# Optimization experiments

Hardware: AMD Instinct MI355X
Metric: run time of the kernel (lower is better)

Reference implementation:

```python
import jax, jax.numpy as jnp
import numpy as np

CH, KS, PAD = 64, 3, 1
B, H, W = 4, 128, 128
EH, EW = 64, 64
K = KS * KS


def setup_inputs() -> dict:
    key = jax.random.key(0)
    ks = jax.random.split(key, 10)
    C = CH
    z = lambda *s: jnp.zeros(s, jnp.float32)
    return {
        "ev_feat": jax.random.normal(ks[0], (B, C, EH, EW), jnp.float32),
        "im_feat": jax.random.normal(ks[1], (B, C, H, W), jnp.float32),
        "mlp_w0": jax.random.normal(ks[2], (2 * C + 4, C), jnp.float32) * 0.05,
        "mlp_b0": z(C),
        "mlp_w1": jax.random.normal(ks[3], (C, C), jnp.float32) * 0.05,
        "mlp_b1": z(C),
        "mlp_w2": jax.random.normal(ks[4], (C, C), jnp.float32) * 0.05,
        "mlp_b2": z(C),
        "mlp_w3": jax.random.normal(ks[5], (C, C), jnp.float32) * 0.05,
        "mlp_b3": z(C),
        "off_w": jax.random.normal(ks[6], (3 * K, C, KS, KS), jnp.float32) * 0.01,
        "off_b": z(3 * K),
        "dcn_w": jax.random.normal(ks[7], (C, C, KS, KS), jnp.float32) * 0.05,
        "dcn_b": z(C),
    }


def _conv(x, w, b):
    y = jax.lax.conv_general_dilated(x, w, (1, 1), [(PAD, PAD), (PAD, PAD)],
                                     dimension_numbers=("NCHW", "OIHW", "NCHW"))
    return y + b[None, :, None, None]


def _forward(ev_feat, im_feat, mlp_w0, mlp_b0, mlp_w1, mlp_b1, mlp_w2, mlp_b2,
             mlp_w3, mlp_b3, off_w, off_b, dcn_w, dcn_b):
    C = CH
    Bn = im_feat.shape[0]
    Q = H * W
    # ---- coordinate-conditioned MLP: LIIF-style nearest query of ev_feat ----
    ys = -1.0 + (2.0 * jnp.arange(H, dtype=jnp.float32) + 1.0) / H  # pixel centers in [-1,1]
    xs = -1.0 + (2.0 * jnp.arange(W, dtype=jnp.float32) + 1.0) / W
    gy, gx = jnp.meshgrid(ys, xs, indexing="ij")
    coord = jnp.stack([gy, gx], -1).reshape(-1, 2)  # (Q,2) as (y,x), torch make_coord order
    iy = jnp.clip(jnp.round(((coord[:, 0] + 1.0) * EH - 1.0) / 2.0), 0, EH - 1).astype(jnp.int32)
    ix = jnp.clip(jnp.round(((coord[:, 1] + 1.0) * EW - 1.0) / 2.0), 0, EW - 1).astype(jnp.int32)
    q_feat = ev_feat[:, :, iy, ix].transpose(0, 2, 1)  # (B,Q,C) nearest-sampled event feature
    q_coord = jnp.stack([-1.0 + (2.0 * iy + 1.0) / EH, -1.0 + (2.0 * ix + 1.0) / EW], -1)
    rel = (coord - q_coord) * jnp.array([EH, EW], jnp.float32)  # (Q,2) rel coord scaled by feat res
    rel_cell = jnp.array([2.0 / H * EH, 2.0 / W * EW], jnp.float32)  # cell * feat res
    q_im = im_feat.reshape(Bn, C, Q).transpose(0, 2, 1)  # (B,Q,C); coords are im_feat pixel centers
    inp = jnp.concatenate([q_feat, q_im,
                           jnp.broadcast_to(rel, (Bn, Q, 2)),
                           jnp.broadcast_to(rel_cell, (Bn, Q, 2))], -1)  # (B,Q,2C+4)
    x = jax.nn.relu(inp @ mlp_w0 + mlp_b0)
    x = jax.nn.relu(x @ mlp_w1 + mlp_b1)
    x = jax.nn.relu(x @ mlp_w2 + mlp_b2)
    x = x @ mlp_w3 + mlp_b3  # (B,Q,C)
    feat = x.reshape(Bn, H, W, C).transpose(0, 3, 1, 2)  # (B,C,H,W)
    # ---- ModulatedDeformConvPack (DCNv2) ----
    oo = _conv(feat, off_w, off_b)  # (B,3K,H,W)
    o1, o2, m = oo[:, :K], oo[:, K:2 * K], oo[:, 2 * K:]
    off = jnp.concatenate([o1, o2], 1)  # (B,2K,H,W), interleaved (y,x) per kernel tap
    off_y, off_x = off[:, 0::2], off[:, 1::2]  # (B,K,H,W)
    mask = jax.nn.sigmoid(m)  # (B,K,H,W)
    ky = (jnp.arange(K) // KS - PAD).astype(jnp.float32)
    kx = (jnp.arange(K) % KS - PAD).astype(jnp.float32)
    py = jnp.arange(H, dtype=jnp.float32)[None, :, None] + ky[:, None, None] + off_y  # (B,K,H,W)
    px = jnp.arange(W, dtype=jnp.float32)[None, None, :] + kx[:, None, None] + off_x
    y0 = jnp.floor(py)
    x0 = jnp.floor(px)
    ly = py - y0
    lx = px - x0

    def gather(yi, xi):
        valid = (yi >= 0) & (yi <= H - 1) & (xi >= 0) & (xi <= W - 1)
        yc = jnp.clip(yi, 0, H - 1).astype(jnp.int32)
        xc = jnp.clip(xi, 0, W - 1).astype(jnp.int32)
        v = jax.vmap(lambda img, yy, xx: img[:, yy, xx])(feat, yc, xc)  # (B,C,K,H,W)
        return v * valid[:, None].astype(feat.dtype)

    w00 = ((1 - ly) * (1 - lx))[:, None]
    w01 = ((1 - ly) * lx)[:, None]
    w10 = (ly * (1 - lx))[:, None]
    w11 = (ly * lx)[:, None]
    samp = (gather(y0, x0) * w00 + gather(y0, x0 + 1) * w01 +
            gather(y0 + 1, x0) * w10 + gather(y0 + 1, x0 + 1) * w11)  # (B,C,K,H,W)
    samp = samp * mask[:, None]
    out = jnp.einsum("bckhw,ock->bohw", samp, dcn_w.reshape(C, C, K))
    return out + dcn_b[None, :, None, None]


def reference(ev_feat, im_feat, mlp_w0, mlp_b0, mlp_w1, mlp_b1, mlp_w2, mlp_b2,
              mlp_w3, mlp_b3, off_w, off_b, dcn_w, dcn_b):
    return _forward(ev_feat, im_feat, mlp_w0, mlp_b0, mlp_w1, mlp_b1, mlp_w2, mlp_b2,
                    mlp_w3, mlp_b3, off_w, off_b, dcn_w, dcn_b)
```

## Files before the change

### kernel.cpp

```cpp
#include <hip/hip_runtime.h>
#include <math.h>

#define CCH 64
#define HH  128
#define WW  128
#define NB  4
#define NPIX (NB*HH*WW)
#define NWG  (NPIX/64)

__device__ __forceinline__ int swz_block(int bid) {
    return (bid & 7) * (NWG >> 3) + (bid >> 3);
}

__global__ __launch_bounds__(256) void prep_kernel(
    const float* __restrict__ off_w, const float* __restrict__ dcn_w,
    float* __restrict__ offT, float* __restrict__ dcnT)
{
    int idx = blockIdx.x * 256 + threadIdx.x;
    if (idx < 576 * 28) {
        int rc = idx / 28;
        int o  = idx % 28;
        offT[rc * 28 + o] = (o < 27) ? off_w[o * 576 + rc] : 0.0f;
    }
    if (idx < 36864) {
        int o    = idx & 63;
        int rest = idx >> 6;
        int ic   = rest & 63;
        int k    = rest >> 6;
        dcnT[(k * 64 + ic) * 64 + o] = dcn_w[o * 576 + ic * 9 + k];
    }
}

__global__ __launch_bounds__(256) void mlp_kernel(
    const float* __restrict__ ev, const float* __restrict__ im,
    const float* __restrict__ w0, const float* __restrict__ b0,
    const float* __restrict__ w1, const float* __restrict__ b1,
    const float* __restrict__ w2, const float* __restrict__ b2,
    const float* __restrict__ w3, const float* __restrict__ b3,
    float* __restrict__ feat2)
{
    __shared__ float xA[64 * 64];
    __shared__ float xB[64 * 64];
    int tid  = threadIdx.x;
    int cg   = __builtin_amdgcn_readfirstlane(tid >> 6);
    int lane = tid & 63;
    int p = swz_block(blockIdx.x) * 64 + lane;
    int b = p >> 14;
    int q = p & 16383;
    int h = q >> 7;
    int w = q & 127;
    int c0 = cg * 16;

    float acc[16];
#pragma unroll
    for (int j = 0; j < 16; ++j) acc[j] = b0[c0 + j];

    const float* evb = ev + ((b * 64) * 64 + (h >> 1)) * 64 + (w >> 1);
    for (int i = 0; i < 64; ++i) {
        float v = evb[i * 4096];
        const float* wr = w0 + i * 64 + c0;
#pragma unroll
        for (int j = 0; j < 16; ++j) acc[j] = fmaf(v, wr[j], acc[j]);
    }
    const float* imb = im + ((b * 64) * 128 + h) * 128 + w;
    for (int i = 0; i < 64; ++i) {
        float v = imb[i * 16384];
        const float* wr = w0 + (64 + i) * 64 + c0;
#pragma unroll
        for (int j = 0; j < 16; ++j) acc[j] = fmaf(v, wr[j], acc[j]);
    }
    {
        float rely = (h & 1) ? 0.5f : -0.5f;
        float relx = (w & 1) ? 0.5f : -0.5f;
        const float* wr = w0 + 128 * 64 + c0;
#pragma unroll
        for (int j = 0; j < 16; ++j) acc[j] = fmaf(rely, wr[j], acc[j]);
#pragma unroll
        for (int j = 0; j < 16; ++j) acc[j] = fmaf(relx, wr[64 + j], acc[j]);
#pragma unroll
        for (int j = 0; j < 16; ++j) acc[j] += wr[128 + j] + wr[192 + j];
    }
#pragma unroll
    for (int j = 0; j < 16; ++j) xA[(c0 + j) * 64 + lane] = fmaxf(acc[j], 0.0f);
    __syncthreads();

#pragma unroll
    for (int j = 0; j < 16; ++j) acc[j] = b1[c0 + j];
    for (int i = 0; i < 64; ++i) {
        float v = xA[i * 64 + lane];
        const float* wr = w1 + i * 64 + c0;
#pragma unroll
        for (int j = 0; j < 16; ++j) acc[j] = fmaf(v, wr[j], acc[j]);
    }
#pragma unroll
    for (int j = 0; j < 16; ++j) xB[(c0 + j) * 64 + lane] = fmaxf(acc[j], 0.0f);
    __syncthreads();

#pragma unroll
    for (int j = 0; j < 16; ++j) acc[j] = b2[c0 + j];
    for (int i = 0; i < 64; ++i) {
        float v = xB[i * 64 + lane];
        const float* wr = w2 + i * 64 + c0;
#pragma unroll
        for (int j = 0; j < 16; ++j) acc[j] = fmaf(v, wr[j], acc[j]);
    }
#pragma unroll
    for (int j = 0; j < 16; ++j) xA[(c0 + j) * 64 + lane] = fmaxf(acc[j], 0.0f);
    __syncthreads();

#pragma unroll
    for (int j = 0; j < 16; ++j) acc[j] = b3[c0 + j];
    for (int i = 0; i < 64; ++i) {
        float v = xA[i * 64 + lane];
        const float* wr = w3 + i * 64 + c0;
#pragma unroll
        for (int j = 0; j < 16; ++j) acc[j] = fmaf(v, wr[j], acc[j]);
    }
    float4* f4 = (float4*)(feat2 + ((b * 16384 + q) * 64 + c0));
#pragma unroll
    for (int j = 0; j < 4; ++j)
        f4[j] = make_float4(acc[4 * j], acc[4 * j + 1], acc[4 * j + 2], acc[4 * j + 3]);
}

__global__ __launch_bounds__(256) void off_kernel(
    const float* __restrict__ feat2, const float* __restrict__ offT,
    const float* __restrict__ off_b,
    float* __restrict__ oo)
{
    __shared__ float po[4 * 27 * 64];
    int tid  = threadIdx.x;
    int wv   = __builtin_amdgcn_readfirstlane(tid >> 6);
    int lane = tid & 63;
    int p = swz_block(blockIdx.x) * 64 + lane;
    int b = p >> 14;
    int q = p & 16383;
    int h = q >> 7;
    int w = q & 127;
    int c0 = wv * 16;

    float acc[27];
#pragma unroll
    for (int o = 0; o < 27; ++o) acc[o] = 0.0f;

    const float* f2 = feat2 + (b * 16384) * 64 + c0;
#pragma unroll 3
    for (int kk = 0; kk < 9; ++kk) {
        int y = h + kk / 3 - 1, x = w + kk % 3 - 1;
        bool ok = (y >= 0) && (y < 128) && (x >= 0) && (x < 128);
        int yc = min(max(y, 0), 127), xc = min(max(x, 0), 127);
        const float4* fp = (const float4*)(f2 + (yc * 128 + xc) * 64);
        float4 v0 = fp[0], v1 = fp[1], v2 = fp[2], v3 = fp[3];
        float zz = ok ? 1.0f : 0.0f;
        float vv[16] = {v0.x*zz, v0.y*zz, v0.z*zz, v0.w*zz,
                        v1.x*zz, v1.y*zz, v1.z*zz, v1.w*zz,
                        v2.x*zz, v2.y*zz, v2.z*zz, v2.w*zz,
                        v3.x*zz, v3.y*zz, v3.z*zz, v3.w*zz};
#pragma unroll
        for (int i = 0; i < 16; ++i) {
            const float* wr = offT + ((c0 + i) * 9 + kk) * 28;
#pragma unroll
            for (int o = 0; o < 27; ++o) acc[o] = fmaf(vv[i], wr[o], acc[o]);
        }
    }

#pragma unroll
    for (int o = 0; o < 27; ++o) po[(wv * 27 + o) * 64 + lane] = acc[o];
    __syncthreads();

#pragma unroll
    for (int j = 0; j < 7; ++j) {
        int o = wv + 4 * j;
        if (o < 27) {
            float s = off_b[o]
                    + po[o * 64 + lane] + po[(27 + o) * 64 + lane]
                    + po[(54 + o) * 64 + lane] + po[(81 + o) * 64 + lane];
            oo[((b * 27 + o) << 14) + q] = s;
        }
    }
}

__device__ __forceinline__ void dcn_transform(
    const float* oob, int k, int h, int w,
    float& W00, float& W01, float& W10, float& W11,
    int& i00, int& i01, int& i10, int& i11)
{
    float oy = oob[(2 * k) << 14];
    float ox = oob[(2 * k + 1) << 14];
    float ml = 1.0f / (1.0f + expf(-oob[(18 + k) << 14]));
    float py = (float)(h + k / 3 - 1) + oy;
    float px = (float)(w + k % 3 - 1) + ox;

    float y0f = floorf(py), x0f = floorf(px);
    float ly = py - y0f, lx = px - x0f;
    int y0 = (int)y0f, x0 = (int)x0f;

    bool vy0 = (y0f >= 0.0f)        && (y0f <= 127.0f);
    bool vy1 = (y0f + 1.0f >= 0.0f) && (y0f + 1.0f <= 127.0f);
    bool vx0 = (x0f >= 0.0f)        && (x0f <= 127.0f);
    bool vx1 = (x0f + 1.0f >= 0.0f) && (x0f + 1.0f <= 127.0f);

    int yc0 = min(max(y0, 0), 127),     yc1 = min(max(y0 + 1, 0), 127);
    int xc0 = min(max(x0, 0), 127),     xc1 = min(max(x0 + 1, 0), 127);

    W00 = (1.0f - ly) * (1.0f - lx) * ml * ((vy0 && vx0) ? 1.0f : 0.0f);
    W01 = (1.0f - ly) * lx          * ml * ((vy0 && vx1) ? 1.0f : 0.0f);
    W10 = ly * (1.0f - lx)          * ml * ((vy1 && vx0) ? 1.0f : 0.0f);
    W11 = ly * lx                   * ml * ((vy1 && vx1) ? 1.0f : 0.0f);

    i00 = yc0 * 128 + xc0; i01 = yc0 * 128 + xc1;
    i10 = yc1 * 128 + xc0; i11 = yc1 * 128 + xc1;
}

__global__ __launch_bounds__(256) void dcn_kernel(
    const float* __restrict__ feat2,
    const float* __restrict__ oo,
    const float* __restrict__ dcnT, const float* __restrict__ dcn_b,
    float* __restrict__ out)
{
    __shared__ float sA[64 * 64];
    __shared__ float sB[64 * 64];
    int tid  = threadIdx.x;
    int wv   = __builtin_amdgcn_readfirstlane(tid >> 6);
    int lane = tid & 63;
    int p = swz_block(blockIdx.x) * 64 + lane;
    int b = p >> 14;
    int q = p & 16383;
    int h = q >> 7;
    int w = q & 127;
    int c0 = wv * 16;

    float acc[16];
#pragma unroll
    for (int j = 0; j < 16; ++j) acc[j] = dcn_b[c0 + j];

    const float* fb2 = feat2 + (b * 16384) * 64 + c0;
    const float* oob = oo + ((b * 27) << 14) + q;

    {
        float W00, W01, W10, W11; int i00, i01, i10, i11;
        dcn_transform(oob, 0, h, w, W00, W01, W10, W11, i00, i01, i10, i11);
        const float4* p00 = (const float4*)(fb2 + i00 * 64);
        const float4* p01 = (const float4*)(fb2 + i01 * 64);
        const float4* p10 = (const float4*)(fb2 + i10 * 64);
        const float4* p11 = (const float4*)(fb2 + i11 * 64);
#pragma unroll
        for (int g = 0; g < 4; ++g) {
            float4 a = p00[g], bb = p01[g], c = p10[g], d = p11[g];
            sA[(c0 + 4 * g + 0) * 64 + lane] = W00 * a.x + W01 * bb.x + W10 * c.x + W11 * d.x;
            sA[(c0 + 4 * g + 1) * 64 + lane] = W00 * a.y + W01 * bb.y + W10 * c.y + W11 * d.y;
            sA[(c0 + 4 * g + 2) * 64 + lane] = W00 * a.z + W01 * bb.z + W10 * c.z + W11 * d.z;
            sA[(c0 + 4 * g + 3) * 64 + lane] = W00 * a.w + W01 * bb.w + W10 * c.w + W11 * d.w;
        }
    }
    __syncthreads();

    float* cur = sA;
    float* nxt = sB;

    for (int k = 0; k < 9; ++k) {
        bool pre = (k < 8);
        float W00, W01, W10, W11; int i00, i01, i10, i11;
        float4 a0, a1, b0, b1, c0v, c1v, d0, d1;
        const float4 *p00 = nullptr, *p01 = nullptr, *p10 = nullptr, *p11 = nullptr;

        if (pre) {
            dcn_transform(oob, k + 1, h, w, W00, W01, W10, W11, i00, i01, i10, i11);
            p00 = (const float4*)(fb2 + i00 * 64);
            p01 = (const float4*)(fb2 + i01 * 64);
            p10 = (const float4*)(fb2 + i10 * 64);
            p11 = (const float4*)(fb2 + i11 * 64);
            a0 = p00[0]; a1 = p00[1];
            b0 = p01[0]; b1 = p01[1];
            c0v = p10[0]; c1v = p10[1];
            d0 = p11[0]; d1 = p11[1];
        }

        const float* wk = dcnT + (k * 64) * 64 + c0;
#pragma unroll 8
        for (int ic = 0; ic < 32; ++ic) {
            float s = cur[ic * 64 + lane];
            const float* wr = wk + ic * 64;
#pragma unroll
            for (int j = 0; j < 16; ++j) acc[j] = fmaf(s, wr[j], acc[j]);
        }

        if (pre) {
            nxt[(c0 + 0) * 64 + lane] = W00 * a0.x + W01 * b0.x + W10 * c0v.x + W11 * d0.x;
            nxt[(c0 + 1) * 64 + lane] = W00 * a0.y + W01 * b0.y + W10 * c0v.y + W11 * d0.y;
            nxt[(c0 + 2) * 64 + lane] = W00 * a0.z + W01 * b0.z + W10 * c0v.z + W11 * d0.z;
            nxt[(c0 + 3) * 64 + lane] = W00 * a0.w + W01 * b0.w + W10 * c0v.w + W11 * d0.w;
            nxt[(c0 + 4) * 64 + lane] = W00 * a1.x + W01 * b1.x + W10 * c1v.x + W11 * d1.x;
            nxt[(c0 + 5) * 64 + lane] = W00 * a1.y + W01 * b1.y + W10 * c1v.y + W11 * d1.y;
            nxt[(c0 + 6) * 64 + lane] = W00 * a1.z + W01 * b1.z + W10 * c1v.z + W11 * d1.z;
            nxt[(c0 + 7) * 64 + lane] = W00 * a1.w + W01 * b1.w + W10 * c1v.w + W11 * d1.w;
            a0 = p00[2]; a1 = p00[3];
            b0 = p01[2]; b1 = p01[3];
            c0v = p10[2]; c1v = p10[3];
            d0 = p11[2]; d1 = p11[3];
        }

#pragma unroll 8
        for (int ic = 32; ic < 64; ++ic) {
            float s = cur[ic * 64 + lane];
            const float* wr = wk + ic * 64;
#pragma unroll
            for (int j = 0; j < 16; ++j) acc[j] = fmaf(s, wr[j], acc[j]);
        }

        if (pre) {
            nxt[(c0 +  8) * 64 + lane] = W00 * a0.x + W01 * b0.x + W10 * c0v.x + W11 * d0.x;
            nxt[(c0 +  9) * 64 + lane] = W00 * a0.y + W01 * b0.y + W10 * c0v.y + W11 * d0.y;
            nxt[(c0 + 10) * 64 + lane] = W00 * a0.z + W01 * b0.z + W10 * c0v.z + W11 * d0.z;
            nxt[(c0 + 11) * 64 + lane] = W00 * a0.w + W01 * b0.w + W10 * c0v.w + W11 * d0.w;
            nxt[(c0 + 12) * 64 + lane] = W00 * a1.x + W01 * b1.x + W10 * c1v.x + W11 * d1.x;
            nxt[(c0 + 13) * 64 + lane] = W00 * a1.y + W01 * b1.y + W10 * c1v.y + W11 * d1.y;
            nxt[(c0 + 14) * 64 + lane] = W00 * a1.z + W01 * b1.z + W10 * c1v.z + W11 * d1.z;
            nxt[(c0 + 15) * 64 + lane] = W00 * a1.w + W01 * b1.w + W10 * c1v.w + W11 * d1.w;
        }

        __syncthreads();
        float* t = cur; cur = nxt; nxt = t;
    }

    float* ob = out + (b * 64 + c0) * 16384 + q;
#pragma unroll
    for (int j = 0; j < 16; ++j) ob[j * 16384] = acc[j];
}

extern "C" void kernel_launch(void* const* d_in, const int* in_sizes, int n_in,
                              void* d_out, int out_size, void* d_ws, size_t ws_size,
                              hipStream_t stream)
{
    const float* ev    = (const float*)d_in[0];
    const float* im    = (const float*)d_in[1];
    const float* w0    = (const float*)d_in[2];
    const float* b0    = (const float*)d_in[3];
    const float* w1    = (const float*)d_in[4];
    const float* b1    = (const float*)d_in[5];
    const float* w2    = (const float*)d_in[6];
    const float* b2    = (const float*)d_in[7];
    const float* w3    = (const float*)d_in[8];
    const float* b3    = (const float*)d_in[9];
    const float* off_w = (const float*)d_in[10];
    const float* off_b = (const float*)d_in[11];
    const float* dcn_w = (const float*)d_in[12];
    const float* dcn_b = (const float*)d_in[13];
    float* out = (float*)d_out;

    char* ws = (char*)d_ws;
    float* feat2 = (float*)(ws);
    float* oo    = (float*)(ws + 16777216);
    float* offT  = (float*)(ws + 23855104);
    float* dcnT  = (float*)(ws + 23920640);

    prep_kernel<<<144, 256, 0, stream>>>(off_w, dcn_w, offT, dcnT);
    mlp_kernel<<<NWG, 256, 0, stream>>>(ev, im, w0, b0, w1, b1, w2, b2,
                                        w3, b3, feat2);
    off_kernel<<<NWG, 256, 0, stream>>>(feat2, offT, off_b, oo);
    dcn_kernel<<<NWG, 256, 0, stream>>>(feat2, oo, dcnT, dcn_b, out);
}
```

Before: 184.8 us.

## Fuse offset conv and deformable conv into one kernel with LDS-held offsets

Merges the offset convolution kernel and the DCN kernel into a single kernel. The 27 offset/mask channels per pixel now stay in shared memory instead of making a round trip through a global buffer, which also removes one launch. The kernel reuses one LDS array for the partial sums and the double-buffered sample tiles, and adds launch_bounds(256,4). The inner DCN loop now loads 16 LDS samples into registers before issuing the FMAs, which raises register pressure.

Result: slower. 526.5 us (+184.9%).

```diff
diff --git a/kernel.cpp b/kernel.cpp
--- a/kernel.cpp
+++ b/kernel.cpp
@@ -122,12 +122,48 @@
         f4[j] = make_float4(acc[4 * j], acc[4 * j + 1], acc[4 * j + 2], acc[4 * j + 3]);
 }
 
-__global__ __launch_bounds__(256) void off_kernel(
-    const float* __restrict__ feat2, const float* __restrict__ offT,
-    const float* __restrict__ off_b,
-    float* __restrict__ oo)
-{
-    __shared__ float po[4 * 27 * 64];
+__device__ __forceinline__ void dcn_transform_r(
+    float oy, float ox, float mlraw, int k, int h, int w,
+    float& W00, float& W01, float& W10, float& W11,
+    int& i00, int& i01, int& i10, int& i11)
+{
+    float ml = 1.0f / (1.0f + expf(-mlraw));
+    float py = (float)(h + k / 3 - 1) + oy;
+    float px = (float)(w + k % 3 - 1) + ox;
+
+    float y0f = floorf(py), x0f = floorf(px);
+    float ly = py - y0f, lx = px - x0f;
+    int y0 = (int)y0f, x0 = (int)x0f;
+
+    bool vy0 = (y0f >= 0.0f)        && (y0f <= 127.0f);
+    bool vy1 = (y0f + 1.0f >= 0.0f) && (y0f + 1.0f <= 127.0f);
+    bool vx0 = (x0f >= 0.0f)        && (x0f <= 127.0f);
+    bool vx1 = (x0f + 1.0f >= 0.0f) && (x0f + 1.0f <= 127.0f);
+
+    int yc0 = min(max(y0, 0), 127),     yc1 = min(max(y0 + 1, 0), 127);
+    int xc0 = min(max(x0, 0), 127),     xc1 = min(max(x0 + 1, 0), 127);
+
+    W00 = (1.0f - ly) * (1.0f - lx) * ml * ((vy0 && vx0) ? 1.0f : 0.0f);
+    W01 = (1.0f - ly) * lx          * ml * ((vy0 && vx1) ? 1.0f : 0.0f);
+    W10 = ly * (1.0f - lx)          * ml * ((vy1 && vx0) ? 1.0f : 0.0f);
+    W11 = ly * lx                   * ml * ((vy1 && vx1) ? 1.0f : 0.0f);
+
+    i00 = yc0 * 128 + xc0; i01 = yc0 * 128 + xc1;
+    i10 = yc1 * 128 + xc0; i11 = yc1 * 128 + xc1;
+}
+
+__global__ __launch_bounds__(256, 4) void fused_kernel(
+    const float* __restrict__ feat2,
+    const float* __restrict__ offT, const float* __restrict__ off_b,
+    const float* __restrict__ dcnT, const float* __restrict__ dcn_b,
+    float* __restrict__ out)
+{
+    __shared__ float lds[9920];
+    float* po  = lds;
+    float* sA  = lds;
+    float* sB  = lds + 4096;
+    float* ool = lds + 8192;
+
     int tid  = threadIdx.x;
     int wv   = __builtin_amdgcn_readfirstlane(tid >> 6);
     int lane = tid & 63;
@@ -138,33 +174,35 @@
     int w = q & 127;
     int c0 = wv * 16;
 
-    float acc[27];
-#pragma unroll
-    for (int o = 0; o < 27; ++o) acc[o] = 0.0f;
-
-    const float* f2 = feat2 + (b * 16384) * 64 + c0;
+    const float* fb2 = feat2 + (b * 16384) * 64 + c0;
+
+    {
+        float acc[27];
+#pragma unroll
+        for (int o = 0; o < 27; ++o) acc[o] = 0.0f;
+
 #pragma unroll 3
-    for (int kk = 0; kk < 9; ++kk) {
-        int y = h + kk / 3 - 1, x = w + kk % 3 - 1;
-        bool ok = (y >= 0) && (y < 128) && (x >= 0) && (x < 128);
-        int yc = min(max(y, 0), 127), xc = min(max(x, 0), 127);
-        const float4* fp = (const float4*)(f2 + (yc * 128 + xc) * 64);
-        float4 v0 = fp[0], v1 = fp[1], v2 = fp[2], v3 = fp[3];
-        float zz = ok ? 1.0f : 0.0f;
-        float vv[16] = {v0.x*zz, v0.y*zz, v0.z*zz, v0.w*zz,
-                        v1.x*zz, v1.y*zz, v1.z*zz, v1.w*zz,
-                        v2.x*zz, v2.y*zz, v2.z*zz, v2.w*zz,
-                        v3.x*zz, v3.y*zz, v3.z*zz, v3.w*zz};
-#pragma unroll
-        for (int i = 0; i < 16; ++i) {
-            const float* wr = offT + ((c0 + i) * 9 + kk) * 28;
-#pragma unroll
-            for (int o = 0; o < 27; ++o) acc[o] = fmaf(vv[i], wr[o], acc[o]);
-        }
-    }
-
-#pragma unroll
-    for (int o = 0; o < 27; ++o) po[(wv * 27 + o) * 64 + lane] = acc[o];
+        for (int kk = 0; kk < 9; ++kk) {
+            int y = h + kk / 3 - 1, x = w + kk % 3 - 1;
+            bool ok = (y >= 0) && (y < 128) && (x >= 0) && (x < 128);
+            int yc = min(max(y, 0), 127), xc = min(max(x, 0), 127);
+            const float4* fp = (const float4*)(fb2 + (yc * 128 + xc) * 64);
+            float4 v0 = fp[0], v1 = fp[1], v2 = fp[2], v3 = fp[3];
+            float zz = ok ? 1.0f : 0.0f;
+            float vv[16] = {v0.x*zz, v0.y*zz, v0.z*zz, v0.w*zz,
+                            v1.x*zz, v1.y*zz, v1.z*zz, v1.w*zz,
+                            v2.x*zz, v2.y*zz, v2.z*zz, v2.w*zz,
+                            v3.x*zz, v3.y*zz, v3.z*zz, v3.w*zz};
+#pragma unroll
+            for (int i = 0; i < 16; ++i) {
+                const float* wr = offT + ((c0 + i) * 9 + kk) * 28;
+#pragma unroll
+                for (int o = 0; o < 27; ++o) acc[o] = fmaf(vv[i], wr[o], acc[o]);
+            }
+        }
+#pragma unroll
+        for (int o = 0; o < 27; ++o) po[(wv * 27 + o) * 64 + lane] = acc[o];
+    }
     __syncthreads();
 
 #pragma unroll
@@ -174,71 +212,21 @@
             float s = off_b[o]
                     + po[o * 64 + lane] + po[(27 + o) * 64 + lane]
                     + po[(54 + o) * 64 + lane] + po[(81 + o) * 64 + lane];
-            oo[((b * 27 + o) << 14) + q] = s;
-        }
-    }
-}
-
-__device__ __forceinline__ void dcn_transform(
-    const float* oob, int k, int h, int w,
-    float& W00, float& W01, float& W10, float& W11,
-    int& i00, int& i01, int& i10, int& i11)
-{
-    float oy = oob[(2 * k) << 14];
-    float ox = oob[(2 * k + 1) << 14];
-    float ml = 1.0f / (1.0f + expf(-oob[(18 + k) << 14]));
-    float py = (float)(h + k / 3 - 1) + oy;
-    float px = (float)(w + k % 3 - 1) + ox;
-
-    float y0f = floorf(py), x0f = floorf(px);
-    float ly = py - y0f, lx = px - x0f;
-    int y0 = (int)y0f, x0 = (int)x0f;
-
-    bool vy0 = (y0f >= 0.0f)        && (y0f <= 127.0f);
-    bool vy1 = (y0f + 1.0f >= 0.0f) && (y0f + 1.0f <= 127.0f);
-    bool vx0 = (x0f >= 0.0f)        && (x0f <= 127.0f);
-    bool vx1 = (x0f + 1.0f >= 0.0f) && (x0f + 1.0f <= 127.0f);
-
-    int yc0 = min(max(y0, 0), 127),     yc1 = min(max(y0 + 1, 0), 127);
-    int xc0 = min(max(x0, 0), 127),     xc1 = min(max(x0 + 1, 0), 127);
-
-    W00 = (1.0f - ly) * (1.0f - lx) * ml * ((vy0 && vx0) ? 1.0f : 0.0f);
-    W01 = (1.0f - ly) * lx          * ml * ((vy0 && vx1) ? 1.0f : 0.0f);
-    W10 = ly * (1.0f - lx)          * ml * ((vy1 && vx0) ? 1.0f : 0.0f);
-    W11 = ly * lx                   * ml * ((vy1 && vx1) ? 1.0f : 0.0f);
-
-    i00 = yc0 * 128 + xc0; i01 = yc0 * 128 + xc1;
-    i10 = yc1 * 128 + xc0; i11 = yc1 * 128 + xc1;
-}
-
-__global__ __launch_bounds__(256) void dcn_kernel(
-    const float* __restrict__ feat2,
-    const float* __restrict__ oo,
-    const float* __restrict__ dcnT, const float* __restrict__ dcn_b,
-    float* __restrict__ out)
-{
-    __shared__ float sA[64 * 64];
-    __shared__ float sB[64 * 64];
-    int tid  = threadIdx.x;
-    int wv   = __builtin_amdgcn_readfirstlane(tid >> 6);
-    int lane = tid & 63;
-    int p = swz_block(blockIdx.x) * 64 + lane;
-    int b = p >> 14;
-    int q = p & 16383;
-    int h = q >> 7;
-    int w = q & 127;
-    int c0 = wv * 16;
+            ool[o * 64 + lane] = s;
+        }
+    }
+    __syncthreads();
 
     float acc[16];
 #pragma unroll
     for (int j = 0; j < 16; ++j) acc[j] = dcn_b[c0 + j];
 
-    const float* fb2 = feat2 + (b * 16384) * 64 + c0;
-    const float* oob = oo + ((b * 27) << 14) + q;
-
     {
+        float oy = ool[(0) * 64 + lane];
+        float ox = ool[(1) * 64 + lane];
+        float om = ool[(18) * 64 + lane];
         float W00, W01, W10, W11; int i00, i01, i10, i11;
-        dcn_transform(oob, 0, h, w, W00, W01, W10, W11, i00, i01, i10, i11);
+        dcn_transform_r(oy, ox, om, 0, h, w, W00, W01, W10, W11, i00, i01, i10, i11);
         const float4* p00 = (const float4*)(fb2 + i00 * 64);
         const float4* p01 = (const float4*)(fb2 + i01 * 64);
         const float4* p10 = (const float4*)(fb2 + i10 * 64);
@@ -252,6 +240,9 @@
             sA[(c0 + 4 * g + 3) * 64 + lane] = W00 * a.w + W01 * bb.w + W10 * c.w + W11 * d.w;
         }
     }
+    float oyN = ool[(2) * 64 + lane];
+    float oxN = ool[(3) * 64 + lane];
+    float omN = ool[(19) * 64 + lane];
     __syncthreads();
 
     float* cur = sA;
@@ -264,7 +255,13 @@
         const float4 *p00 = nullptr, *p01 = nullptr, *p10 = nullptr, *p11 = nullptr;
 
         if (pre) {
-            dcn_transform(oob, k + 1, h, w, W00, W01, W10, W11, i00, i01, i10, i11);
+            dcn_transform_r(oyN, oxN, omN, k + 1, h, w,
+                            W00, W01, W10, W11, i00, i01, i10, i11);
+            if (k < 7) {
+                oyN = ool[(2 * (k + 2)) * 64 + lane];
+                oxN = ool[(2 * (k + 2) + 1) * 64 + lane];
+                omN = ool[(18 + (k + 2)) * 64 + lane];
+            }
             p00 = (const float4*)(fb2 + i00 * 64);
             p01 = (const float4*)(fb2 + i01 * 64);
             p10 = (const float4*)(fb2 + i10 * 64);
@@ -276,12 +273,17 @@
         }
 
         const float* wk = dcnT + (k * 64) * 64 + c0;
-#pragma unroll 8
-        for (int ic = 0; ic < 32; ++ic) {
-            float s = cur[ic * 64 + lane];
-            const float* wr = wk + ic * 64;
-#pragma unroll
-            for (int j = 0; j < 16; ++j) acc[j] = fmaf(s, wr[j], acc[j]);
+#pragma unroll
+        for (int cch = 0; cch < 2; ++cch) {
+            float sreg[16];
+#pragma unroll
+            for (int i = 0; i < 16; ++i) sreg[i] = cur[(cch * 16 + i) * 64 + lane];
+#pragma unroll
+            for (int i = 0; i < 16; ++i) {
+                const float* wr = wk + (cch * 16 + i) * 64;
+#pragma unroll
+                for (int j = 0; j < 16; ++j) acc[j] = fmaf(sreg[i], wr[j], acc[j]);
+            }
         }
 
         if (pre) {
@@ -299,12 +301,17 @@
             d0 = p11[2]; d1 = p11[3];
         }
 
-#pragma unroll 8
-        for (int ic = 32; ic < 64; ++ic) {
-            float s = cur[ic * 64 + lane];
-            const float* wr = wk + ic * 64;
-#pragma unroll
-            for (int j = 0; j < 16; ++j) acc[j] = fmaf(s, wr[j], acc[j]);
+#pragma unroll
+        for (int cch = 2; cch < 4; ++cch) {
+            float sreg[16];
+#pragma unroll
+            for (int i = 0; i < 16; ++i) sreg[i] = cur[(cch * 16 + i) * 64 + lane];
+#pragma unroll
+            for (int i = 0; i < 16; ++i) {
+                const float* wr = wk + (cch * 16 + i) * 64;
+#pragma unroll
+                for (int j = 0; j < 16; ++j) acc[j] = fmaf(sreg[i], wr[j], acc[j]);
+            }
         }
 
         if (pre) {
@@ -349,13 +356,11 @@
 
     char* ws = (char*)d_ws;
     float* feat2 = (float*)(ws);
-    float* oo    = (float*)(ws + 16777216);
     float* offT  = (float*)(ws + 23855104);
     float* dcnT  = (float*)(ws + 23920640);
 
     prep_kernel<<<144, 256, 0, stream>>>(off_w, dcn_w, offT, dcnT);
     mlp_kernel<<<NWG, 256, 0, stream>>>(ev, im, w0, b0, w1, b1, w2, b2,
                                         w3, b3, feat2);
-    off_kernel<<<NWG, 256, 0, stream>>>(feat2, offT, off_b, oo);
-    dcn_kernel<<<NWG, 256, 0, stream>>>(feat2, oo, dcnT, dcn_b, out);
-}
+    fused_kernel<<<NWG, 256, 0, stream>>>(feat2, offT, off_b, dcnT, dcn_b, out);
+}
```
